# Optimization experiments

Hardware: AMD Instinct MI355X
Metric: run time of the kernel (lower is better)

Reference implementation:

```python
import jax, jax.numpy as jnp
import numpy as np

B, CLEN, QLEN, H = 32, 384, 64, 768


def _p(key, shape, scale=0.02):
    return jax.random.normal(key, shape, dtype=jnp.float32) * scale


def setup_inputs() -> dict:
    key = jax.random.key(0)
    ks = iter(jax.random.split(key, 64))
    d = {}
    d["c"] = jax.random.normal(next(ks), (B, CLEN, H), jnp.float32)
    d["q"] = jax.random.normal(next(ks), (B, QLEN, H), jnp.float32)
    d["w_att_c"] = _p(next(ks), (H,)); d["b_att_c"] = jnp.zeros((), jnp.float32)
    d["w_att_q"] = _p(next(ks), (H,)); d["b_att_q"] = jnp.zeros((), jnp.float32)
    d["w_att_cq"] = _p(next(ks), (H,)); d["b_att_cq"] = jnp.zeros((), jnp.float32)
    def add_lstm(prefix, in_dim):
        for dr in ("f", "b"):
            d[prefix + dr + "_wih"] = _p(next(ks), (4 * H, in_dim))
            d[prefix + dr + "_whh"] = _p(next(ks), (4 * H, H))
            d[prefix + dr + "_b"] = jnp.zeros((4 * H,), jnp.float32)  # b_ih + b_hh fused
    add_lstm("l1", 4 * H)  # modeling_LSTM1: input 4H
    add_lstm("l2", 2 * H)  # modeling_LSTM2: input 2H
    add_lstm("lo", 2 * H)  # output_LSTM: input 2H
    d["p1_wg"] = _p(next(ks), (4 * H,)); d["p1_bg"] = jnp.zeros((), jnp.float32)
    d["p1_wm"] = _p(next(ks), (2 * H,)); d["p1_bm"] = jnp.zeros((), jnp.float32)
    d["p2_wg"] = _p(next(ks), (4 * H,)); d["p2_bg"] = jnp.zeros((), jnp.float32)
    d["p2_wm"] = _p(next(ks), (2 * H,)); d["p2_bm"] = jnp.zeros((), jnp.float32)
    return d


def _lstm_dir(x, wih, whh, b):
    # single-direction LSTM, torch gate order (i, f, g, o)
    Bb, T, _ = x.shape
    Hh = whh.shape[1]
    xg = jnp.einsum("bti,gi->btg", x, wih) + b  # precompute input projections [B,T,4H]
    def step(carry, xt):
        h, cst = carry
        g = xt + h @ whh.T
        i, f, gg, o = jnp.split(g, 4, axis=-1)
        i = jax.nn.sigmoid(i); f = jax.nn.sigmoid(f)
        gg = jnp.tanh(gg); o = jax.nn.sigmoid(o)
        cst = f * cst + i * gg
        h = o * jnp.tanh(cst)
        return (h, cst), h
    init = (jnp.zeros((Bb, Hh), x.dtype), jnp.zeros((Bb, Hh), x.dtype))
    _, hs = jax.lax.scan(step, init, jnp.swapaxes(xg, 0, 1))
    return jnp.swapaxes(hs, 0, 1)


def _bilstm(x, fwih, fwhh, fb, bwih, bwhh, bb):
    hf = _lstm_dir(x, fwih, fwhh, fb)
    hb = _lstm_dir(x[:, ::-1], bwih, bwhh, bb)[:, ::-1]
    return jnp.concatenate([hf, hb], axis=-1)


def _forward(c, q,
             w_att_c, b_att_c, w_att_q, b_att_q, w_att_cq, b_att_cq,
             l1f_wih, l1f_whh, l1f_b, l1b_wih, l1b_whh, l1b_b,
             l2f_wih, l2f_whh, l2f_b, l2b_wih, l2b_whh, l2b_b,
             lof_wih, lof_whh, lof_b, lob_wih, lob_whh, lob_b,
             p1_wg, p1_bg, p1_wm, p1_bm, p2_wg, p2_bg, p2_wm, p2_bm):
    # --- att_flow_layer: trilinear similarity collapsed to a single einsum ---
    # original loops over q_len applying att_weight_cq(c * q_i); equivalent to:
    cq = jnp.einsum("bih,bjh,h->bij", c, q, w_att_cq) + b_att_cq  # [B,C,Q]
    s = (c @ w_att_c + b_att_c)[:, :, None] + (q @ w_att_q + b_att_q)[:, None, :] + cq
    a = jax.nn.softmax(s, axis=2)                       # attend context->query
    c2q = jnp.einsum("bij,bjh->bih", a, q)              # [B,C,H]
    b_w = jax.nn.softmax(jnp.max(s, axis=2), axis=1)    # [B,C]
    q2c = jnp.einsum("bi,bih->bh", b_w, c)[:, None, :]  # [B,1,H]
    g = jnp.concatenate([c, c2q, c * c2q, c * q2c], axis=-1)  # [B,C,8H? no, 4H]

    # --- modeling layers (two stacked biLSTMs) ---
    m1 = _bilstm(g, l1f_wih, l1f_whh, l1f_b, l1b_wih, l1b_whh, l1b_b)
    m = _bilstm(m1, l2f_wih, l2f_whh, l2f_b, l2b_wih, l2b_whh, l2b_b)

    # --- output layer ---
    p1 = (g @ p1_wg + p1_bg) + (m @ p1_wm + p1_bm)      # [B,C]
    m2 = _bilstm(m, lof_wih, lof_whh, lof_b, lob_wih, lob_whh, lob_b)
    p2 = (g @ p2_wg + p2_bg) + (m2 @ p2_wm + p2_bm)
    return p1, p2


def reference(c, q,
              w_att_c, b_att_c, w_att_q, b_att_q, w_att_cq, b_att_cq,
              l1f_wih, l1f_whh, l1f_b, l1b_wih, l1b_whh, l1b_b,
              l2f_wih, l2f_whh, l2f_b, l2b_wih, l2b_whh, l2b_b,
              lof_wih, lof_whh, lof_b, lob_wih, lob_whh, lob_b,
              p1_wg, p1_bg, p1_wm, p1_bm, p2_wg, p2_bg, p2_wm, p2_bm):
    return _forward(c, q,
                    w_att_c, b_att_c, w_att_q, b_att_q, w_att_cq, b_att_cq,
                    l1f_wih, l1f_whh, l1f_b, l1b_wih, l1b_whh, l1b_b,
                    l2f_wih, l2f_whh, l2f_b, l2b_wih, l2b_whh, l2b_b,
                    lof_wih, lof_whh, lof_b, lob_wih, lob_whh, lob_b,
                    p1_wg, p1_bg, p1_wm, p1_bm, p2_wg, p2_bg, p2_wm, p2_bm)
```

## Files before the change

### kernel.cpp

```cpp
#include <hip/hip_runtime.h>


typedef __bf16 bf16_t;
typedef __bf16 bf16x4 __attribute__((ext_vector_type(4)));
typedef __bf16 bf16x8 __attribute__((ext_vector_type(8)));
typedef float  f32x4  __attribute__((ext_vector_type(4)));
typedef unsigned long long ull;

#define TT 384

__device__ __forceinline__ void gload_lds16(const void* g, void* l) {
  __builtin_amdgcn_global_load_lds((const __attribute__((address_space(1))) void*)g,
                                   (__attribute__((address_space(3))) void*)l, 16, 0, 0);
}

__global__ void k_zeroE(unsigned* p) {
  int i = blockIdx.x * 256 + threadIdx.x;
  __hip_atomic_store(p + i, 0xFFFF0000u, __ATOMIC_RELAXED, __HIP_MEMORY_SCOPE_AGENT);
}

template<int BN, int EPI, int BSRC>
__global__ __launch_bounds__(256) void k_gemm(
    const bf16_t* __restrict__ A, const void* __restrict__ Bv, const void* __restrict__ Bv2,
    int nsplit, void* __restrict__ Cv,
    int M, int N, int K, long sAb, long sBb, long sCb,
    const float* __restrict__ rowb, const float* __restrict__ colb,
    const float* __restrict__ sb)
{
  constexpr int BM = 128, BK = 32;
  constexpr int NT = BN / 32;
  __shared__ bf16_t sA[BM * BK];
  __shared__ bf16_t sB[BN * BK];
  const int t    = threadIdx.x;
  const int lane = t & 63;
  const int wm   = (t >> 6) >> 1, wn = (t >> 6) & 1;
  const long bz  = blockIdx.z;
  const int nbase = blockIdx.y * BN;
  const bf16_t* Ab = A + bz * sAb + (long)blockIdx.x * BM * K;
  const bf16_t* Bb = nullptr;
  const float*  Bf = nullptr;
  if constexpr (BSRC == 0)
    Bb = (const bf16_t*)Bv + bz * sBb + (long)nbase * K;
  else
    Bf = (nbase < nsplit) ? ((const float*)Bv  + (long)nbase * K)
                          : ((const float*)Bv2 + (long)(nbase - nsplit) * K);

  const int r4 = t >> 2;
  const int kq = (t & 3) ^ ((r4 >> 1) & 3);

  f32x4 acc[4][NT];
  #pragma unroll
  for (int i = 0; i < 4; i++)
    #pragma unroll
    for (int j = 0; j < NT; j++) acc[i][j] = (f32x4){0.f, 0.f, 0.f, 0.f};

  const int mrow = lane & 15;
  const int fq   = lane >> 4;
  const int aswz = (fq ^ ((mrow >> 1) & 3)) * 8;

  for (int k0 = 0; k0 < K; k0 += BK) {
    __syncthreads();
    gload_lds16(Ab + (long)r4 * K + k0 + kq * 8,        (char*)sA + t * 16);
    gload_lds16(Ab + (long)(64 + r4) * K + k0 + kq * 8, (char*)sA + 4096 + t * 16);
    if constexpr (BSRC == 0) {
      gload_lds16(Bb + (long)r4 * K + k0 + kq * 8,        (char*)sB + t * 16);
      if constexpr (BN == 128)
        gload_lds16(Bb + (long)(64 + r4) * K + k0 + kq * 8, (char*)sB + 4096 + t * 16);
    } else {
      {
        f32x4 b0 = *(const f32x4*)(Bf + (long)r4 * K + k0 + kq * 8);
        f32x4 b1 = *(const f32x4*)(Bf + (long)r4 * K + k0 + kq * 8 + 4);
        bf16x8 bb;
        #pragma unroll
        for (int e = 0; e < 4; e++) { bb[e] = (bf16_t)b0[e]; bb[e + 4] = (bf16_t)b1[e]; }
        *(bf16x8*)((char*)sB + t * 16) = bb;
      }
      if constexpr (BN == 128) {
        f32x4 b0 = *(const f32x4*)(Bf + (long)(64 + r4) * K + k0 + kq * 8);
        f32x4 b1 = *(const f32x4*)(Bf + (long)(64 + r4) * K + k0 + kq * 8 + 4);
        bf16x8 bb;
        #pragma unroll
        for (int e = 0; e < 4; e++) { bb[e] = (bf16_t)b0[e]; bb[e + 4] = (bf16_t)b1[e]; }
        *(bf16x8*)((char*)sB + 4096 + t * 16) = bb;
      }
    }
    __syncthreads();

    bf16x8 af[4], bv[NT];
    #pragma unroll
    for (int mt = 0; mt < 4; mt++)
      af[mt] = *(const bf16x8*)(sA + (wm * 64 + mt * 16 + mrow) * 32 + aswz);
    #pragma unroll
    for (int nt = 0; nt < NT; nt++)
      bv[nt] = *(const bf16x8*)(sB + (wn * (BN / 2) + nt * 16 + mrow) * 32 + aswz);
    #pragma unroll
    for (int mt = 0; mt < 4; mt++)
      #pragma unroll
      for (int nt = 0; nt < NT; nt++)
        acc[mt][nt] = __builtin_amdgcn_mfma_f32_16x16x32_bf16(af[mt], bv[nt], acc[mt][nt], 0, 0, 0);
  }

  const int rbase = (lane >> 4) * 4;
  #pragma unroll
  for (int mt = 0; mt < 4; mt++)
    #pragma unroll
    for (int nt = 0; nt < NT; nt++)
      #pragma unroll
      for (int r = 0; r < 4; r++) {
        int grow = blockIdx.x * BM + wm * 64 + mt * 16 + rbase + r;
        int gcol = nbase + wn * (BN / 2) + nt * 16 + (lane & 15);
        if constexpr (EPI == 0) {
          ((bf16_t*)Cv)[bz * sCb + (long)grow * N + gcol] = (bf16_t)acc[mt][nt][r];
        } else {
          ((float*)Cv)[bz * sCb + (long)grow * N + gcol] =
              acc[mt][nt][r] + rowb[bz * M + grow] + colb[bz * N + gcol] + sb[0];
        }
      }
}

__global__ __launch_bounds__(512) void k_lstm(
    const bf16_t* __restrict__ xg, bf16_t* __restrict__ mout,
    unsigned* __restrict__ E,
    const float* __restrict__ whh_f, const float* __restrict__ whh_b,
    const float* __restrict__ bias_f, const float* __restrict__ bias_b,
    int tagbase)
{
  __shared__ bf16_t sH[16 * 776];
  __shared__ float  sG[4 * 544];
  const int t    = threadIdx.x;
  const int lane = t & 63;
  const int w    = t >> 6;
  const int g    = w & 3;
  const int ch   = w >> 2;
  const int blk  = blockIdx.x;
  const int dir  = blk / 48;
  const int qq   = blk - dir * 48;
  const int sl   = qq >> 1;
  const int bg   = qq & 1;
  const int j0   = sl * 32;
  const float* whh  = dir ? whh_b : whh_f;
  const float* bias = dir ? bias_b : bias_f;

  const int mrow = lane & 15;
  const int fq   = lane >> 4;

  bf16x8 bw[24];
  {
    const float* wrow = whh + (long)(g * 768 + j0 + ch * 16 + mrow) * 768 + fq * 8;
    #pragma unroll
    for (int kc = 0; kc < 24; kc++) {
      f32x4 v0 = *(const f32x4*)(wrow + kc * 32);
      f32x4 v1 = *(const f32x4*)(wrow + kc * 32 + 4);
      bf16x8 bb;
      #pragma unroll
      for (int e = 0; e < 4; e++) { bb[e] = (bf16_t)v0[e]; bb[e + 4] = (bf16_t)v1[e]; }
      bw[kc] = bb;
    }
  }

  const int b16 = t >> 5;
  const int jj  = t & 31;
  float bsv[4];
  #pragma unroll
  for (int gi = 0; gi < 4; gi++) bsv[gi] = bias[gi * 768 + j0 + jj];

  int soff[12];
  #pragma unroll
  for (int i = 0; i < 12; i++) {
    int e = i * 512 + t;
    soff[i] = (e / 384) * 1552 + (e % 384) * 4;
  }

  float cst = 0.f;
  const int aoff0 = mrow * 776 + fq * 8;
  const long xrow0 = (long)(bg * 16 + b16) * TT;

  for (int s = 0; s < TT; s++) {
    const int tc = dir ? (TT - 1 - s) : s;

    float xv[4];
    {
      long xr = (xrow0 + tc) * 6144 + dir * 3072 + j0 + jj;
      #pragma unroll
      for (int gi = 0; gi < 4; gi++) xv[gi] = (float)xg[xr + gi * 768];
    }

    if (s == 0) {
      for (int e = t; e < 1552; e += 512)
        *(f32x4*)((char*)sH + e * 16) = (f32x4){0.f, 0.f, 0.f, 0.f};
    } else {
      const unsigned want = (unsigned)(tagbase + s - 1);
      const int par = (s - 1) & 1;
      const ull* src = (const ull*)E + ((long)(par * 2 + dir) * 32 + bg * 16) * 384;
      ull qv[12];
      #pragma unroll
      for (int i = 0; i < 12; i++)
        qv[i] = __hip_atomic_load(src + i * 512 + t, __ATOMIC_RELAXED, __HIP_MEMORY_SCOPE_AGENT);
      for (;;) {
        unsigned bad = 0;
        #pragma unroll
        for (int i = 0; i < 12; i++) {
          unsigned lo = (unsigned)qv[i], hi = (unsigned)(qv[i] >> 32);
          if ((lo >> 16) != want || (hi >> 16) != want) bad |= 1u << i;
        }
        if (!bad) break;
        #pragma unroll
        for (int i = 0; i < 12; i++)
          if (bad & (1u << i))
            qv[i] = __hip_atomic_load(src + i * 512 + t, __ATOMIC_RELAXED, __HIP_MEMORY_SCOPE_AGENT);
      }
      #pragma unroll
      for (int i = 0; i < 12; i++) {
        ushort2 hh;
        hh.x = (unsigned short)qv[i];
        hh.y = (unsigned short)(qv[i] >> 32);
        *(ushort2*)((char*)sH + soff[i]) = hh;
      }
    }
    __syncthreads();

    f32x4 a0 = (f32x4){0.f, 0.f, 0.f, 0.f};
    f32x4 a1 = (f32x4){0.f, 0.f, 0.f, 0.f};
    #pragma unroll
    for (int kc = 0; kc < 24; kc += 2) {
      bf16x8 av0 = *(const bf16x8*)(sH + aoff0 + kc * 32);
      bf16x8 av1 = *(const bf16x8*)(sH + aoff0 + kc * 32 + 32);
      a0 = __builtin_amdgcn_mfma_f32_16x16x32_bf16(av0, bw[kc],     a0, 0, 0, 0);
      a1 = __builtin_amdgcn_mfma_f32_16x16x32_bf16(av1, bw[kc + 1], a1, 0, 0, 0);
    }
    #pragma unroll
    for (int r = 0; r < 4; r++)
      sG[g * 544 + (ch * 16 + mrow) * 17 + fq * 4 + r] = a0[r] + a1[r];
    __syncthreads();

    {
      float gi = sG[0 * 544 + jj * 17 + b16] + xv[0] + bsv[0];
      float gf = sG[1 * 544 + jj * 17 + b16] + xv[1] + bsv[1];
      float gg = sG[2 * 544 + jj * 17 + b16] + xv[2] + bsv[2];
      float go = sG[3 * 544 + jj * 17 + b16] + xv[3] + bsv[3];
      gi = 1.f / (1.f + __expf(-gi));
      gf = 1.f / (1.f + __expf(-gf));
      gg = 1.f - 2.f / (__expf(2.f * gg) + 1.f);
      go = 1.f / (1.f + __expf(-go));
      cst = gf * cst + gi * gg;
      float hv = go * (1.f - 2.f / (__expf(2.f * cst) + 1.f));
      union { bf16_t b; unsigned short u; } pk;
      pk.b = (bf16_t)hv;
      unsigned tag = (unsigned)(tagbase + s);
      long ed = ((long)((s & 1) * 2 + dir) * 32 + bg * 16 + b16) * 768 + j0 + jj;
      __hip_atomic_store(E + ed, (tag << 16) | pk.u,
                         __ATOMIC_RELAXED, __HIP_MEMORY_SCOPE_AGENT);
      mout[(xrow0 + tc) * 1536 + dir * 768 + j0 + jj] = pk.b;
    }
  }
}


__global__ __launch_bounds__(256) void k_pack(
    const float* __restrict__ c, const float* __restrict__ q,
    const float* __restrict__ wcq, bf16_t* __restrict__ cw, bf16_t* __restrict__ qb)
{
  int i = blockIdx.x * 256 + threadIdx.x;
  if (i < 9437184) {
    int h = i % 768;
    cw[i] = (bf16_t)(c[i] * wcq[h]);
  } else {
    int j = i - 9437184;
    qb[j] = (bf16_t)q[j];
  }
}

__global__ __launch_bounds__(256) void k_proj(
    const float* __restrict__ c, const float* __restrict__ q,
    const float* __restrict__ wc, const float* __restrict__ bc,
    const float* __restrict__ wq, const float* __restrict__ bq,
    float* __restrict__ projc, float* __restrict__ projq)
{
  int row  = blockIdx.x * 4 + (threadIdx.x >> 6);
  int lane = threadIdx.x & 63;
  const float *src, *w;
  bool isC = row < 12288;
  if (isC) { src = c + (long)row * 768;          w = wc; }
  else     { src = q + (long)(row - 12288) * 768; w = wq; }
  float a = 0.f;
  for (int k = lane * 4; k < 768; k += 256) {
    f32x4 v = *(const f32x4*)(src + k);
    f32x4 wv = *(const f32x4*)(w + k);
    a += v[0]*wv[0] + v[1]*wv[1] + v[2]*wv[2] + v[3]*wv[3];
  }
  for (int m = 32; m; m >>= 1) a += __shfl_xor(a, m);
  if (lane == 0) {
    if (isC) projc[row] = a + bc[0];
    else     projq[row - 12288] = a + bq[0];
  }
}

__global__ __launch_bounds__(256) void k_smax_j(
    const float* __restrict__ s, bf16_t* __restrict__ a, float* __restrict__ smax)
{
  int row  = blockIdx.x * 4 + (threadIdx.x >> 6);
  int lane = threadIdx.x & 63;
  float v = s[(long)row * 64 + lane];
  float mx = v;
  for (int m = 32; m; m >>= 1) mx = fmaxf(mx, __shfl_xor(mx, m));
  float p = __expf(v - mx);
  float sum = p;
  for (int m = 32; m; m >>= 1) sum += __shfl_xor(sum, m);
  a[(long)row * 64 + lane] = (bf16_t)(p / sum);
  if (lane == 0) smax[row] = mx;
}

__global__ __launch_bounds__(384) void k_smax_i(
    const float* __restrict__ smax, float* __restrict__ bw)
{
  __shared__ float red[8];
  int b = blockIdx.x, t = threadIdx.x;
  int lane = t & 63, wv = t >> 6;
  float v = smax[b * 384 + t];
  float mx = v;
  for (int m = 32; m; m >>= 1) mx = fmaxf(mx, __shfl_xor(mx, m));
  if (lane == 0) red[wv] = mx;
  __syncthreads();
  float gm = red[0];
  #pragma unroll
  for (int i = 1; i < 6; i++) gm = fmaxf(gm, red[i]);
  float p = __expf(v - gm);
  float sm = p;
  for (int m = 32; m; m >>= 1) sm += __shfl_xor(sm, m);
  __syncthreads();
  if (lane == 0) red[wv] = sm;
  __syncthreads();
  float tot = red[0];
  #pragma unroll
  for (int i = 1; i < 6; i++) tot += red[i];
  bw[b * 384 + t] = p / tot;
}

__global__ __launch_bounds__(256) void k_q2c(
    const float* __restrict__ bw, const float* __restrict__ c, float* __restrict__ q2c)
{
  int b = blockIdx.y;
  int h = blockIdx.x * 256 + threadIdx.x;
  const float* cb = c + (long)b * 384 * 768;
  float acc = 0.f;
  for (int i = 0; i < 384; i++) acc += bw[b * 384 + i] * cb[(long)i * 768 + h];
  q2c[b * 768 + h] = acc;
}

__global__ __launch_bounds__(256) void k_tq(
    const bf16_t* __restrict__ qb, bf16_t* __restrict__ qT)
{
  __shared__ bf16_t sT[64][72];
  int b = blockIdx.y, hc = blockIdx.x, t = threadIdx.x;
  {
    int j = t >> 2, h0 = (t & 3) * 16;
    const bf16_t* src = qb + (long)(b * 64 + j) * 768 + hc * 64 + h0;
    *(bf16x8*)&sT[j][h0]     = *(const bf16x8*)(src);
    *(bf16x8*)&sT[j][h0 + 8] = *(const bf16x8*)(src + 8);
  }
  __syncthreads();
  {
    int h = t >> 2, j0 = (t & 3) * 16;
    bf16x8 o0, o1;
    #pragma unroll
    for (int e = 0; e < 8; e++) { o0[e] = sT[j0 + e][h]; o1[e] = sT[j0 + 8 + e][h]; }
    bf16_t* dst = qT + (long)(b * 768 + hc * 64 + h) * 64 + j0;
    *(bf16x8*)dst       = o0;
    *(bf16x8*)(dst + 8) = o1;
  }
}

__global__ __launch_bounds__(256) void k_buildg(
    const float* __restrict__ c, const bf16_t* __restrict__ c2q,
    const float* __restrict__ q2c, bf16_t* __restrict__ g)
{
  int i = blockIdx.x * 256 + threadIdx.x;
  int h = i % 768;
  int row = i / 768;
  int b = row / 384;
  float cv  = c[i];
  float cqv = (float)c2q[i];
  float qcv = q2c[b * 768 + h];
  bf16_t* gr = g + (long)row * 3072;
  gr[h]        = (bf16_t)cv;
  gr[768 + h]  = c2q[i];
  gr[1536 + h] = (bf16_t)(cv * cqv);
  gr[2304 + h] = (bf16_t)(cv * qcv);
}

__global__ __launch_bounds__(256) void k_headsg(
    const bf16_t* __restrict__ g, const float* __restrict__ w1, const float* __restrict__ w2,
    float* __restrict__ pg1, float* __restrict__ pg2)
{
  int row  = blockIdx.x * 4 + (threadIdx.x >> 6);
  int lane = threadIdx.x & 63;
  float a1 = 0.f, a2 = 0.f;
  const bf16_t* gr = g + (long)row * 3072;
  for (int k = lane * 8; k < 3072; k += 512) {
    bf16x8 v = *(const bf16x8*)(gr + k);
    f32x4 wa = *(const f32x4*)(w1 + k), wb = *(const f32x4*)(w1 + k + 4);
    f32x4 xa = *(const f32x4*)(w2 + k), xb = *(const f32x4*)(w2 + k + 4);
    #pragma unroll
    for (int e = 0; e < 4; e++) {
      a1 += (float)v[e] * wa[e] + (float)v[e + 4] * wb[e];
      a2 += (float)v[e] * xa[e] + (float)v[e + 4] * xb[e];
    }
  }
  for (int m_ = 32; m_; m_ >>= 1) { a1 += __shfl_xor(a1, m_); a2 += __shfl_xor(a2, m_); }
  if (lane == 0) { pg1[row] = a1; pg2[row] = a2; }
}

__global__ __launch_bounds__(256) void k_headsm(
    const bf16_t* __restrict__ m, const float* __restrict__ wm,
    const float* __restrict__ pg, const float* __restrict__ bg,
    const float* __restrict__ bm, float* __restrict__ out)
{
  int row  = blockIdx.x * 4 + (threadIdx.x >> 6);
  int lane = threadIdx.x & 63;
  float a = 0.f;
  const bf16_t* mr = m + (long)row * 1536;
  for (int k = lane * 8; k < 1536; k += 512) {
    bf16x8 v = *(const bf16x8*)(mr + k);
    f32x4 wa = *(const f32x4*)(wm + k), wb = *(const f32x4*)(wm + k + 4);
    #pragma unroll
    for (int e = 0; e < 4; e++) a += (float)v[e] * wa[e] + (float)v[e + 4] * wb[e];
  }
  for (int m_ = 32; m_; m_ >>= 1) a += __shfl_xor(a, m_);
  if (lane == 0) out[row] = pg[row] + a + bg[0] + bm[0];
}


extern "C" void kernel_launch(void* const* d_in, const int* in_sizes, int n_in,
                              void* d_out, int out_size, void* d_ws, size_t ws_size,
                              hipStream_t stream)
{
  (void)in_sizes; (void)n_in; (void)out_size; (void)ws_size;
  const float* c    = (const float*)d_in[0];
  const float* q    = (const float*)d_in[1];
  const float* wac  = (const float*)d_in[2];
  const float* bac  = (const float*)d_in[3];
  const float* waq  = (const float*)d_in[4];
  const float* baq  = (const float*)d_in[5];
  const float* wacq = (const float*)d_in[6];
  const float* bacq = (const float*)d_in[7];
  const float* l1f_wih = (const float*)d_in[8];
  const float* l1f_whh = (const float*)d_in[9];
  const float* l1f_b   = (const float*)d_in[10];
  const float* l1b_wih = (const float*)d_in[11];
  const float* l1b_whh = (const float*)d_in[12];
  const float* l1b_b   = (const float*)d_in[13];
  const float* l2f_wih = (const float*)d_in[14];
  const float* l2f_whh = (const float*)d_in[15];
  const float* l2f_b   = (const float*)d_in[16];
  const float* l2b_wih = (const float*)d_in[17];
  const float* l2b_whh = (const float*)d_in[18];
  const float* l2b_b   = (const float*)d_in[19];
  const float* lof_wih = (const float*)d_in[20];
  const float* lof_whh = (const float*)d_in[21];
  const float* lof_b   = (const float*)d_in[22];
  const float* lob_wih = (const float*)d_in[23];
  const float* lob_whh = (const float*)d_in[24];
  const float* lob_b   = (const float*)d_in[25];
  const float* p1wg = (const float*)d_in[26];
  const float* p1bg = (const float*)d_in[27];
  const float* p1wm = (const float*)d_in[28];
  const float* p1bm = (const float*)d_in[29];
  const float* p2wg = (const float*)d_in[30];
  const float* p2bg = (const float*)d_in[31];
  const float* p2wm = (const float*)d_in[32];
  const float* p2bm = (const float*)d_in[33];

  char* ws = (char*)d_ws;
  bf16_t* g_bf = (bf16_t*)ws;
  bf16_t* mA   = (bf16_t*)ws;
  bf16_t* mB   = (bf16_t*)(ws + 37748736L);
  bf16_t* m2   = (bf16_t*)ws;
  char*   xgc  = ws + 75497472L;
  bf16_t* xg   = (bf16_t*)xgc;
  bf16_t* cw  = (bf16_t*)xgc;
  bf16_t* qb  = (bf16_t*)(xgc + 18874368L);
  bf16_t* qT  = (bf16_t*)(xgc + 22020096L);
  float*  sS  = (float*) (xgc + 25165824L);
  bf16_t* aP  = (bf16_t*)(xgc + 28311552L);
  bf16_t* c2q = (bf16_t*)(xgc + 29884416L);
  char* tail = ws + 226492416L;
  float*    projc = (float*)tail;
  float*    projq = (float*)(tail + 49152);
  float*    smax  = (float*)(tail + 57344);
  float*    bw    = (float*)(tail + 106496);
  float*    q2c   = (float*)(tail + 155648);
  float*    pg1   = (float*)(tail + 253952);
  float*    pg2   = (float*)(tail + 303104);
  unsigned* E     = (unsigned*)(tail + 352256);

  k_zeroE<<<768, 256, 0, stream>>>(E);

  k_pack<<<43008, 256, 0, stream>>>(c, q, wacq, cw, qb);
  k_proj<<<3584, 256, 0, stream>>>(c, q, wac, bac, waq, baq, projc, projq);
  k_gemm<64,1,0><<<dim3(3,1,32), 256, 0, stream>>>(cw, qb, nullptr, 1<<30, sS,
      384, 64, 768, (long)384*768, (long)64*768, (long)384*64, projc, projq, bacq);
  k_smax_j<<<3072, 256, 0, stream>>>(sS, aP, smax);
  k_smax_i<<<32, 384, 0, stream>>>(smax, bw);
  k_q2c<<<dim3(3,32), 256, 0, stream>>>(bw, c, q2c);
  k_tq<<<dim3(12,32), 256, 0, stream>>>(qb, qT);
  k_gemm<64,0,0><<<dim3(3,12,32), 256, 0, stream>>>(aP, qT, nullptr, 1<<30, c2q,
      384, 768, 64, (long)384*64, (long)768*64, (long)384*768, nullptr, nullptr, nullptr);
  k_buildg<<<36864, 256, 0, stream>>>(c, c2q, q2c, g_bf);
  k_headsg<<<3072, 256, 0, stream>>>(g_bf, p1wg, p2wg, pg1, pg2);

  k_gemm<128,0,1><<<dim3(96,48,1), 256, 0, stream>>>(g_bf, l1f_wih, l1b_wih, 3072, xg,
      12288, 6144, 3072, 0, 0, 0, nullptr, nullptr, nullptr);
  k_lstm<<<96, 512, 0, stream>>>(xg, mA, E, l1f_whh, l1b_whh, l1f_b, l1b_b, 0);

  k_gemm<128,0,1><<<dim3(96,48,1), 256, 0, stream>>>(mA, l2f_wih, l2b_wih, 3072, xg,
      12288, 6144, 1536, 0, 0, 0, nullptr, nullptr, nullptr);
  k_lstm<<<96, 512, 0, stream>>>(xg, mB, E, l2f_whh, l2b_whh, l2f_b, l2b_b, 384);
  k_headsm<<<3072, 256, 0, stream>>>(mB, p1wm, pg1, p1bg, p1bm, (float*)d_out);

  k_gemm<128,0,1><<<dim3(96,48,1), 256, 0, stream>>>(mB, lof_wih, lob_wih, 3072, xg,
      12288, 6144, 1536, 0, 0, 0, nullptr, nullptr, nullptr);
  k_lstm<<<96, 512, 0, stream>>>(xg, m2, E, lof_whh, lob_whh, lof_b, lob_b, 768);
  k_headsm<<<3072, 256, 0, stream>>>(m2, p2wm, pg2, p2bg, p2bm, (float*)d_out + 12288);
}
```

Measured before the change: 6.563 ms.

## Interleave four direction/batch-group LSTM phases per block with prefetched handoff loads

Result: slower. 10.66 ms (+62.5%).

```diff
diff --git a/kernel.cpp b/kernel.cpp
--- a/kernel.cpp
+++ b/kernel.cpp
@@ -12,6 +12,12 @@
 __device__ __forceinline__ void gload_lds16(const void* g, void* l) {
   __builtin_amdgcn_global_load_lds((const __attribute__((address_space(1))) void*)g,
                                    (__attribute__((address_space(3))) void*)l, 16, 0, 0);
+}
+
+__device__ __forceinline__ void wg_barrier_lds() {
+  asm volatile("s_waitcnt lgkmcnt(0)" ::: "memory");
+  __builtin_amdgcn_s_barrier();
+  asm volatile("" ::: "memory");
 }
 
 __global__ void k_zeroE(unsigned* p) {
@@ -118,6 +124,88 @@
       }
 }
 
+
+#define LSTM_PHASE(D, BGc, CST, QV, ID, IB, IPAR)                                  \
+  {                                                                                \
+    const int tc = (D) ? (TT - 1 - s) : s;                                         \
+    float xv0 = 0.f, xv1 = 0.f, xv2 = 0.f, xv3 = 0.f;                              \
+    if (t < 256) {                                                                 \
+      long xr = ((long)((BGc) * 16 + b16e) * TT + tc) * 6144 + (D) * 3072 + j0 + jje; \
+      xv0 = (float)xg[xr];        xv1 = (float)xg[xr + 768];                       \
+      xv2 = (float)xg[xr + 1536]; xv3 = (float)xg[xr + 2304];                      \
+    }                                                                              \
+    if (s == 0) {                                                                  \
+      if ((D) == 0 && (BGc) == 0) {                                                \
+        for (int e = t; e < 1552; e += 512)                                        \
+          *(f32x4*)((char*)sH + e * 16) = (f32x4){0.f, 0.f, 0.f, 0.f};             \
+      }                                                                            \
+    } else {                                                                       \
+      const unsigned want = (unsigned)(tagbase + s - 1);                           \
+      const ull* rsrc = (const ull*)E + ((long)(((s - 1) & 1) * 2 + (D)) * 32 + (BGc) * 16) * 384; \
+      for (;;) {                                                                   \
+        unsigned bad = 0;                                                          \
+        _Pragma("unroll")                                                          \
+        for (int i = 0; i < 12; i++) {                                             \
+          unsigned lo = (unsigned)QV[i], hi = (unsigned)(QV[i] >> 32);             \
+          if ((lo >> 16) != want || (hi >> 16) != want) bad |= 1u << i;            \
+        }                                                                          \
+        if (!bad) break;                                                           \
+        _Pragma("unroll")                                                          \
+        for (int i = 0; i < 12; i++)                                               \
+          if (bad & (1u << i))                                                     \
+            QV[i] = __hip_atomic_load(rsrc + i * 512 + t, __ATOMIC_RELAXED, __HIP_MEMORY_SCOPE_AGENT); \
+      }                                                                            \
+      _Pragma("unroll")                                                            \
+      for (int i = 0; i < 12; i++) {                                               \
+        ushort2 hh;                                                                \
+        hh.x = (unsigned short)QV[i];                                              \
+        hh.y = (unsigned short)(QV[i] >> 32);                                      \
+        *(ushort2*)((char*)sH + soff[i]) = hh;                                     \
+      }                                                                            \
+    }                                                                              \
+    {                                                                              \
+      const ull* isrc = (const ull*)E + ((long)((IPAR) * 2 + (ID)) * 32 + (IB) * 16) * 384; \
+      _Pragma("unroll")                                                            \
+      for (int i = 0; i < 12; i++)                                                 \
+        QV[i] = __hip_atomic_load(isrc + i * 512 + t, __ATOMIC_RELAXED, __HIP_MEMORY_SCOPE_AGENT); \
+    }                                                                              \
+    wg_barrier_lds();                                                              \
+    if (wd == (D)) {                                                               \
+      f32x4 a0 = (f32x4){0.f, 0.f, 0.f, 0.f};                                      \
+      f32x4 a1 = (f32x4){0.f, 0.f, 0.f, 0.f};                                      \
+      _Pragma("unroll")                                                            \
+      for (int kc = 0; kc < 24; kc += 2) {                                         \
+        bf16x8 av0 = *(const bf16x8*)(sH + aoff0 + kc * 32);                       \
+        bf16x8 av1 = *(const bf16x8*)(sH + aoff0 + kc * 32 + 32);                  \
+        a0 = __builtin_amdgcn_mfma_f32_16x16x32_bf16(av0, bw[kc],     a0, 0, 0, 0);\
+        a1 = __builtin_amdgcn_mfma_f32_16x16x32_bf16(av1, bw[kc + 1], a1, 0, 0, 0);\
+      }                                                                            \
+      _Pragma("unroll")                                                            \
+      for (int r = 0; r < 4; r++)                                                  \
+        sG[g * 272 + mrow * 17 + fq * 4 + r] = a0[r] + a1[r];                      \
+    }                                                                              \
+    wg_barrier_lds();                                                              \
+    if (t < 256) {                                                                 \
+      float gv0 = sG[0 * 272 + jje * 17 + b16e] + xv0 + ((D) ? bsb0 : bsf0);       \
+      float gv1 = sG[1 * 272 + jje * 17 + b16e] + xv1 + ((D) ? bsb1 : bsf1);       \
+      float gv2 = sG[2 * 272 + jje * 17 + b16e] + xv2 + ((D) ? bsb2 : bsf2);       \
+      float gv3 = sG[3 * 272 + jje * 17 + b16e] + xv3 + ((D) ? bsb3 : bsf3);       \
+      gv0 = 1.f / (1.f + __expf(-gv0));                                            \
+      gv1 = 1.f / (1.f + __expf(-gv1));                                            \
+      gv2 = 1.f - 2.f / (__expf(2.f * gv2) + 1.f);                                 \
+      gv3 = 1.f / (1.f + __expf(-gv3));                                            \
+      CST = gv1 * CST + gv0 * gv2;                                                 \
+      float hv = gv3 * (1.f - 2.f / (__expf(2.f * CST) + 1.f));                    \
+      union { bf16_t b; unsigned short u; } pk;                                    \
+      pk.b = (bf16_t)hv;                                                           \
+      unsigned tag = (unsigned)(tagbase + s);                                      \
+      long ed = ((long)((s & 1) * 2 + (D)) * 32 + (BGc) * 16 + b16e) * 768 + j0 + jje; \
+      __hip_atomic_store(E + ed, (tag << 16) | pk.u,                               \
+                         __ATOMIC_RELAXED, __HIP_MEMORY_SCOPE_AGENT);              \
+      mout[((long)((BGc) * 16 + b16e) * TT + tc) * 1536 + (D) * 768 + j0 + jje] = pk.b; \
+    }                                                                              \
+  }
+
 __global__ __launch_bounds__(512) void k_lstm(
     const bf16_t* __restrict__ xg, bf16_t* __restrict__ mout,
     unsigned* __restrict__ E,
@@ -126,27 +214,22 @@
     int tagbase)
 {
   __shared__ bf16_t sH[16 * 776];
-  __shared__ float  sG[4 * 544];
+  __shared__ float  sG[4 * 272];
   const int t    = threadIdx.x;
   const int lane = t & 63;
   const int w    = t >> 6;
   const int g    = w & 3;
-  const int ch   = w >> 2;
-  const int blk  = blockIdx.x;
-  const int dir  = blk / 48;
-  const int qq   = blk - dir * 48;
-  const int sl   = qq >> 1;
-  const int bg   = qq & 1;
-  const int j0   = sl * 32;
-  const float* whh  = dir ? whh_b : whh_f;
-  const float* bias = dir ? bias_b : bias_f;
-
+  const int wd   = w >> 2;
+  const int j0   = blockIdx.x * 16;
   const int mrow = lane & 15;
   const int fq   = lane >> 4;
-
+  const int jje  = t & 15;
+  const int b16e = (t >> 4) & 15;
+
+  const float* whh = wd ? whh_b : whh_f;
   bf16x8 bw[24];
   {
-    const float* wrow = whh + (long)(g * 768 + j0 + ch * 16 + mrow) * 768 + fq * 8;
+    const float* wrow = whh + (long)(g * 768 + j0 + mrow) * 768 + fq * 8;
     #pragma unroll
     for (int kc = 0; kc < 24; kc++) {
       f32x4 v0 = *(const f32x4*)(wrow + kc * 32);
@@ -158,11 +241,14 @@
     }
   }
 
-  const int b16 = t >> 5;
-  const int jj  = t & 31;
-  float bsv[4];
-  #pragma unroll
-  for (int gi = 0; gi < 4; gi++) bsv[gi] = bias[gi * 768 + j0 + jj];
+  const float bsf0 = bias_f[0 * 768 + j0 + jje];
+  const float bsf1 = bias_f[1 * 768 + j0 + jje];
+  const float bsf2 = bias_f[2 * 768 + j0 + jje];
+  const float bsf3 = bias_f[3 * 768 + j0 + jje];
+  const float bsb0 = bias_b[0 * 768 + j0 + jje];
+  const float bsb1 = bias_b[1 * 768 + j0 + jje];
+  const float bsb2 = bias_b[2 * 768 + j0 + jje];
+  const float bsb3 = bias_b[3 * 768 + j0 + jje];
 
   int soff[12];
   #pragma unroll
@@ -171,87 +257,16 @@
     soff[i] = (e / 384) * 1552 + (e % 384) * 4;
   }
 
-  float cst = 0.f;
   const int aoff0 = mrow * 776 + fq * 8;
-  const long xrow0 = (long)(bg * 16 + b16) * TT;
+
+  float cst00 = 0.f, cst01 = 0.f, cst10 = 0.f, cst11 = 0.f;
+  ull qvA[12] = {}, qvB[12] = {};
 
   for (int s = 0; s < TT; s++) {
-    const int tc = dir ? (TT - 1 - s) : s;
-
-    float xv[4];
-    {
-      long xr = (xrow0 + tc) * 6144 + dir * 3072 + j0 + jj;
-      #pragma unroll
-      for (int gi = 0; gi < 4; gi++) xv[gi] = (float)xg[xr + gi * 768];
-    }
-
-    if (s == 0) {
-      for (int e = t; e < 1552; e += 512)
-        *(f32x4*)((char*)sH + e * 16) = (f32x4){0.f, 0.f, 0.f, 0.f};
-    } else {
-      const unsigned want = (unsigned)(tagbase + s - 1);
-      const int par = (s - 1) & 1;
-      const ull* src = (const ull*)E + ((long)(par * 2 + dir) * 32 + bg * 16) * 384;
-      ull qv[12];
-      #pragma unroll
-      for (int i = 0; i < 12; i++)
-        qv[i] = __hip_atomic_load(src + i * 512 + t, __ATOMIC_RELAXED, __HIP_MEMORY_SCOPE_AGENT);
-      for (;;) {
-        unsigned bad = 0;
-        #pragma unroll
-        for (int i = 0; i < 12; i++) {
-          unsigned lo = (unsigned)qv[i], hi = (unsigned)(qv[i] >> 32);
-          if ((lo >> 16) != want || (hi >> 16) != want) bad |= 1u << i;
-        }
-        if (!bad) break;
-        #pragma unroll
-        for (int i = 0; i < 12; i++)
-          if (bad & (1u << i))
-            qv[i] = __hip_atomic_load(src + i * 512 + t, __ATOMIC_RELAXED, __HIP_MEMORY_SCOPE_AGENT);
-      }
-      #pragma unroll
-      for (int i = 0; i < 12; i++) {
-        ushort2 hh;
-        hh.x = (unsigned short)qv[i];
-        hh.y = (unsigned short)(qv[i] >> 32);
-        *(ushort2*)((char*)sH + soff[i]) = hh;
-      }
-    }
-    __syncthreads();
-
-    f32x4 a0 = (f32x4){0.f, 0.f, 0.f, 0.f};
-    f32x4 a1 = (f32x4){0.f, 0.f, 0.f, 0.f};
-    #pragma unroll
-    for (int kc = 0; kc < 24; kc += 2) {
-      bf16x8 av0 = *(const bf16x8*)(sH + aoff0 + kc * 32);
-      bf16x8 av1 = *(const bf16x8*)(sH + aoff0 + kc * 32 + 32);
-      a0 = __builtin_amdgcn_mfma_f32_16x16x32_bf16(av0, bw[kc],     a0, 0, 0, 0);
-      a1 = __builtin_amdgcn_mfma_f32_16x16x32_bf16(av1, bw[kc + 1], a1, 0, 0, 0);
-    }
-    #pragma unroll
-    for (int r = 0; r < 4; r++)
-      sG[g * 544 + (ch * 16 + mrow) * 17 + fq * 4 + r] = a0[r] + a1[r];
-    __syncthreads();
-
-    {
-      float gi = sG[0 * 544 + jj * 17 + b16] + xv[0] + bsv[0];
-      float gf = sG[1 * 544 + jj * 17 + b16] + xv[1] + bsv[1];
-      float gg = sG[2 * 544 + jj * 17 + b16] + xv[2] + bsv[2];
-      float go = sG[3 * 544 + jj * 17 + b16] + xv[3] + bsv[3];
-      gi = 1.f / (1.f + __expf(-gi));
-      gf = 1.f / (1.f + __expf(-gf));
-      gg = 1.f - 2.f / (__expf(2.f * gg) + 1.f);
-      go = 1.f / (1.f + __expf(-go));
-      cst = gf * cst + gi * gg;
-      float hv = go * (1.f - 2.f / (__expf(2.f * cst) + 1.f));
-      union { bf16_t b; unsigned short u; } pk;
-      pk.b = (bf16_t)hv;
-      unsigned tag = (unsigned)(tagbase + s);
-      long ed = ((long)((s & 1) * 2 + dir) * 32 + bg * 16 + b16) * 768 + j0 + jj;
-      __hip_atomic_store(E + ed, (tag << 16) | pk.u,
-                         __ATOMIC_RELAXED, __HIP_MEMORY_SCOPE_AGENT);
-      mout[(xrow0 + tc) * 1536 + dir * 768 + j0 + jj] = pk.b;
-    }
+    LSTM_PHASE(0, 0, cst00, qvA, 1, 0, ((s - 1) & 1))
+    LSTM_PHASE(0, 1, cst01, qvB, 1, 1, ((s - 1) & 1))
+    LSTM_PHASE(1, 0, cst10, qvA, 0, 0, (s & 1))
+    LSTM_PHASE(1, 1, cst11, qvB, 0, 1, (s & 1))
   }
 }
 
@@ -510,15 +525,15 @@
 
   k_gemm<128,0,1><<<dim3(96,48,1), 256, 0, stream>>>(g_bf, l1f_wih, l1b_wih, 3072, xg,
       12288, 6144, 3072, 0, 0, 0, nullptr, nullptr, nullptr);
-  k_lstm<<<96, 512, 0, stream>>>(xg, mA, E, l1f_whh, l1b_whh, l1f_b, l1b_b, 0);
+  k_lstm<<<48, 512, 0, stream>>>(xg, mA, E, l1f_whh, l1b_whh, l1f_b, l1b_b, 0);
 
   k_gemm<128,0,1><<<dim3(96,48,1), 256, 0, stream>>>(mA, l2f_wih, l2b_wih, 3072, xg,
       12288, 6144, 1536, 0, 0, 0, nullptr, nullptr, nullptr);
-  k_lstm<<<96, 512, 0, stream>>>(xg, mB, E, l2f_whh, l2b_whh, l2f_b, l2b_b, 384);
+  k_lstm<<<48, 512, 0, stream>>>(xg, mB, E, l2f_whh, l2b_whh, l2f_b, l2b_b, 384);
   k_headsm<<<3072, 256, 0, stream>>>(mB, p1wm, pg1, p1bg, p1bm, (float*)d_out);
 
   k_gemm<128,0,1><<<dim3(96,48,1), 256, 0, stream>>>(mB, lof_wih, lob_wih, 3072, xg,
       12288, 6144, 1536, 0, 0, 0, nullptr, nullptr, nullptr);
-  k_lstm<<<96, 512, 0, stream>>>(xg, m2, E, lof_whh, lob_whh, lof_b, lob_b, 768);
+  k_lstm<<<48, 512, 0, stream>>>(xg, m2, E, lof_whh, lob_whh, lof_b, lob_b, 768);
   k_headsm<<<3072, 256, 0, stream>>>(m2, p2wm, pg2, p2bg, p2bm, (float*)d_out + 12288);
 }
```

## Halve LSTM block count with 1024-thread blocks, prefetch inputs, pack stores

Applied to the files above, without the earlier changes.

After: 10.51 ms. +60.1%, slower.

```diff
diff --git a/kernel.cpp b/kernel.cpp
--- a/kernel.cpp
+++ b/kernel.cpp
@@ -12,6 +12,12 @@
 __device__ __forceinline__ void gload_lds16(const void* g, void* l) {
   __builtin_amdgcn_global_load_lds((const __attribute__((address_space(1))) void*)g,
                                    (__attribute__((address_space(3))) void*)l, 16, 0, 0);
+}
+
+__device__ __forceinline__ void wg_barrier_lds() {
+  asm volatile("s_waitcnt lgkmcnt(0)" ::: "memory");
+  __builtin_amdgcn_s_barrier();
+  asm volatile("" ::: "memory");
 }
 
 __global__ void k_zeroE(unsigned* p) {
@@ -118,7 +124,7 @@
       }
 }
 
-__global__ __launch_bounds__(512) void k_lstm(
+__global__ __launch_bounds__(1024) void k_lstm(
     const bf16_t* __restrict__ xg, bf16_t* __restrict__ mout,
     unsigned* __restrict__ E,
     const float* __restrict__ whh_f, const float* __restrict__ whh_b,
@@ -126,18 +132,18 @@
     int tagbase)
 {
   __shared__ bf16_t sH[16 * 776];
-  __shared__ float  sG[4 * 544];
+  __shared__ float  sG[4 * 64 * 17];
   const int t    = threadIdx.x;
   const int lane = t & 63;
   const int w    = t >> 6;
   const int g    = w & 3;
   const int ch   = w >> 2;
   const int blk  = blockIdx.x;
-  const int dir  = blk / 48;
-  const int qq   = blk - dir * 48;
+  const int dir  = blk / 24;
+  const int qq   = blk - dir * 24;
   const int sl   = qq >> 1;
   const int bg   = qq & 1;
-  const int j0   = sl * 32;
+  const int j0   = sl * 64;
   const float* whh  = dir ? whh_b : whh_f;
   const float* bias = dir ? bias_b : bias_f;
 
@@ -158,66 +164,77 @@
     }
   }
 
-  const int b16 = t >> 5;
-  const int jj  = t & 31;
+  const int jje  = t & 63;
+  const int b16e = t >> 6;
   float bsv[4];
   #pragma unroll
-  for (int gi = 0; gi < 4; gi++) bsv[gi] = bias[gi * 768 + j0 + jj];
-
-  int soff[12];
+  for (int gi = 0; gi < 4; gi++) bsv[gi] = bias[gi * 768 + j0 + jje];
+
+  int soff[6];
   #pragma unroll
-  for (int i = 0; i < 12; i++) {
-    int e = i * 512 + t;
+  for (int i = 0; i < 6; i++) {
+    int e = i * 1024 + t;
     soff[i] = (e / 384) * 1552 + (e % 384) * 4;
   }
 
   float cst = 0.f;
   const int aoff0 = mrow * 776 + fq * 8;
-  const long xrow0 = (long)(bg * 16 + b16) * TT;
+  const long xrow0 = (long)(bg * 16 + b16e) * TT;
+
+  float xc[4], xn[4];
+  {
+    int tc0 = dir ? (TT - 1) : 0;
+    long xr = (xrow0 + tc0) * 6144 + dir * 3072 + j0 + jje;
+    #pragma unroll
+    for (int gi = 0; gi < 4; gi++) xn[gi] = (float)xg[xr + gi * 768];
+  }
 
   for (int s = 0; s < TT; s++) {
     const int tc = dir ? (TT - 1 - s) : s;
 
-    float xv[4];
+    #pragma unroll
+    for (int gi = 0; gi < 4; gi++) xc[gi] = xn[gi];
     {
-      long xr = (xrow0 + tc) * 6144 + dir * 3072 + j0 + jj;
+      int sn = (s + 1 < TT) ? s + 1 : s;
+      int tcn = dir ? (TT - 1 - sn) : sn;
+      long xr = (xrow0 + tcn) * 6144 + dir * 3072 + j0 + jje;
       #pragma unroll
-      for (int gi = 0; gi < 4; gi++) xv[gi] = (float)xg[xr + gi * 768];
+      for (int gi = 0; gi < 4; gi++) xn[gi] = (float)xg[xr + gi * 768];
     }
 
     if (s == 0) {
-      for (int e = t; e < 1552; e += 512)
+      for (int e = t; e < 1552; e += 1024)
         *(f32x4*)((char*)sH + e * 16) = (f32x4){0.f, 0.f, 0.f, 0.f};
     } else {
       const unsigned want = (unsigned)(tagbase + s - 1);
       const int par = (s - 1) & 1;
       const ull* src = (const ull*)E + ((long)(par * 2 + dir) * 32 + bg * 16) * 384;
-      ull qv[12];
+      ull qv[6];
       #pragma unroll
-      for (int i = 0; i < 12; i++)
-        qv[i] = __hip_atomic_load(src + i * 512 + t, __ATOMIC_RELAXED, __HIP_MEMORY_SCOPE_AGENT);
+      for (int i = 0; i < 6; i++)
+        qv[i] = __hip_atomic_load(src + i * 1024 + t, __ATOMIC_RELAXED, __HIP_MEMORY_SCOPE_AGENT);
       for (;;) {
         unsigned bad = 0;
         #pragma unroll
-        for (int i = 0; i < 12; i++) {
+        for (int i = 0; i < 6; i++) {
           unsigned lo = (unsigned)qv[i], hi = (unsigned)(qv[i] >> 32);
           if ((lo >> 16) != want || (hi >> 16) != want) bad |= 1u << i;
         }
         if (!bad) break;
         #pragma unroll
-        for (int i = 0; i < 12; i++)
+        for (int i = 0; i < 6; i++)
           if (bad & (1u << i))
-            qv[i] = __hip_atomic_load(src + i * 512 + t, __ATOMIC_RELAXED, __HIP_MEMORY_SCOPE_AGENT);
+            qv[i] = __hip_atomic_load(src + i * 1024 + t, __ATOMIC_RELAXED, __HIP_MEMORY_SCOPE_AGENT);
       }
       #pragma unroll
-      for (int i = 0; i < 12; i++) {
+      for (int i = 0; i < 6; i++) {
         ushort2 hh;
         hh.x = (unsigned short)qv[i];
         hh.y = (unsigned short)(qv[i] >> 32);
         *(ushort2*)((char*)sH + soff[i]) = hh;
       }
     }
-    __syncthreads();
+    wg_barrier_lds();
 
     f32x4 a0 = (f32x4){0.f, 0.f, 0.f, 0.f};
     f32x4 a1 = (f32x4){0.f, 0.f, 0.f, 0.f};
@@ -230,27 +247,32 @@
     }
     #pragma unroll
     for (int r = 0; r < 4; r++)
-      sG[g * 544 + (ch * 16 + mrow) * 17 + fq * 4 + r] = a0[r] + a1[r];
-    __syncthreads();
+      sG[g * 1088 + (ch * 16 + mrow) * 17 + fq * 4 + r] = a0[r] + a1[r];
+    wg_barrier_lds();
 
     {
-      float gi = sG[0 * 544 + jj * 17 + b16] + xv[0] + bsv[0];
-      float gf = sG[1 * 544 + jj * 17 + b16] + xv[1] + bsv[1];
-      float gg = sG[2 * 544 + jj * 17 + b16] + xv[2] + bsv[2];
-      float go = sG[3 * 544 + jj * 17 + b16] + xv[3] + bsv[3];
-      gi = 1.f / (1.f + __expf(-gi));
-      gf = 1.f / (1.f + __expf(-gf));
-      gg = 1.f - 2.f / (__expf(2.f * gg) + 1.f);
-      go = 1.f / (1.f + __expf(-go));
-      cst = gf * cst + gi * gg;
-      float hv = go * (1.f - 2.f / (__expf(2.f * cst) + 1.f));
+      float gv0 = sG[0 * 1088 + jje * 17 + b16e] + xc[0] + bsv[0];
+      float gv1 = sG[1 * 1088 + jje * 17 + b16e] + xc[1] + bsv[1];
+      float gv2 = sG[2 * 1088 + jje * 17 + b16e] + xc[2] + bsv[2];
+      float gv3 = sG[3 * 1088 + jje * 17 + b16e] + xc[3] + bsv[3];
+      gv0 = 1.f / (1.f + __expf(-gv0));
+      gv1 = 1.f / (1.f + __expf(-gv1));
+      gv2 = 1.f - 2.f / (__expf(2.f * gv2) + 1.f);
+      gv3 = 1.f / (1.f + __expf(-gv3));
+      cst = gv1 * cst + gv0 * gv2;
+      float hv = gv3 * (1.f - 2.f / (__expf(2.f * cst) + 1.f));
       union { bf16_t b; unsigned short u; } pk;
       pk.b = (bf16_t)hv;
       unsigned tag = (unsigned)(tagbase + s);
-      long ed = ((long)((s & 1) * 2 + dir) * 32 + bg * 16 + b16) * 768 + j0 + jj;
-      __hip_atomic_store(E + ed, (tag << 16) | pk.u,
-                         __ATOMIC_RELAXED, __HIP_MEMORY_SCOPE_AGENT);
-      mout[(xrow0 + tc) * 1536 + dir * 768 + j0 + jj] = pk.b;
+      unsigned myd = (tag << 16) | pk.u;
+      unsigned od  = (unsigned)__shfl_xor((int)myd, 1);
+      if ((t & 1) == 0) {
+        long ed = ((long)((s & 1) * 2 + dir) * 32 + bg * 16 + b16e) * 768 + j0 + jje;
+        __hip_atomic_store((ull*)E + (ed >> 1), (ull)myd | ((ull)od << 32),
+                           __ATOMIC_RELAXED, __HIP_MEMORY_SCOPE_AGENT);
+        unsigned mo = (unsigned)pk.u | ((od & 0xFFFFu) << 16);
+        *(unsigned*)(mout + (xrow0 + tc) * 1536 + dir * 768 + j0 + jje) = mo;
+      }
     }
   }
 }
@@ -510,15 +532,15 @@
 
   k_gemm<128,0,1><<<dim3(96,48,1), 256, 0, stream>>>(g_bf, l1f_wih, l1b_wih, 3072, xg,
       12288, 6144, 3072, 0, 0, 0, nullptr, nullptr, nullptr);
-  k_lstm<<<96, 512, 0, stream>>>(xg, mA, E, l1f_whh, l1b_whh, l1f_b, l1b_b, 0);
+  k_lstm<<<48, 1024, 0, stream>>>(xg, mA, E, l1f_whh, l1b_whh, l1f_b, l1b_b, 0);
 
   k_gemm<128,0,1><<<dim3(96,48,1), 256, 0, stream>>>(mA, l2f_wih, l2b_wih, 3072, xg,
       12288, 6144, 1536, 0, 0, 0, nullptr, nullptr, nullptr);
-  k_lstm<<<96, 512, 0, stream>>>(xg, mB, E, l2f_whh, l2b_whh, l2f_b, l2b_b, 384);
+  k_lstm<<<48, 1024, 0, stream>>>(xg, mB, E, l2f_whh, l2b_whh, l2f_b, l2b_b, 384);
   k_headsm<<<3072, 256, 0, stream>>>(mB, p1wm, pg1, p1bg, p1bm, (float*)d_out);
 
   k_gemm<128,0,1><<<dim3(96,48,1), 256, 0, stream>>>(mB, lof_wih, lob_wih, 3072, xg,
       12288, 6144, 1536, 0, 0, 0, nullptr, nullptr, nullptr);
-  k_lstm<<<96, 512, 0, stream>>>(xg, m2, E, lof_whh, lob_whh, lof_b, lob_b, 768);
+  k_lstm<<<48, 1024, 0, stream>>>(xg, m2, E, lof_whh, lob_whh, lof_b, lob_b, 768);
   k_headsm<<<3072, 256, 0, stream>>>(m2, p2wm, pg2, p2bg, p2bm, (float*)d_out + 12288);
 }
```

## Replace per-element tagged hidden-state exchange with per-wave flags and packed data

Applied to the files above, without the earlier changes.

Result: slower. 8.310 ms (+26.6%).

```diff
diff --git a/kernel.cpp b/kernel.cpp
--- a/kernel.cpp
+++ b/kernel.cpp
@@ -14,9 +14,15 @@
                                    (__attribute__((address_space(3))) void*)l, 16, 0, 0);
 }
 
+__device__ __forceinline__ void wg_barrier_lds() {
+  asm volatile("s_waitcnt lgkmcnt(0)" ::: "memory");
+  __builtin_amdgcn_s_barrier();
+  asm volatile("" ::: "memory");
+}
+
 __global__ void k_zeroE(unsigned* p) {
   int i = blockIdx.x * 256 + threadIdx.x;
-  __hip_atomic_store(p + i, 0xFFFF0000u, __ATOMIC_RELAXED, __HIP_MEMORY_SCOPE_AGENT);
+  __hip_atomic_store(p + i, 0xFFFFFFFFu, __ATOMIC_RELAXED, __HIP_MEMORY_SCOPE_AGENT);
 }
 
 template<int BN, int EPI, int BSRC>
@@ -126,7 +132,7 @@
     int tagbase)
 {
   __shared__ bf16_t sH[16 * 776];
-  __shared__ float  sG[4 * 544];
+  __shared__ float  sG[4 * 272];
   const int t    = threadIdx.x;
   const int lane = t & 63;
   const int w    = t >> 6;
@@ -144,6 +150,9 @@
   const int mrow = lane & 15;
   const int fq   = lane >> 4;
 
+  unsigned* Es = E;
+  unsigned* Ed = E + 1536;
+
   bf16x8 bw[24];
   {
     const float* wrow = whh + (long)(g * 768 + j0 + ch * 16 + mrow) * 768 + fq * 8;
@@ -164,11 +173,11 @@
   #pragma unroll
   for (int gi = 0; gi < 4; gi++) bsv[gi] = bias[gi * 768 + j0 + jj];
 
-  int soff[12];
+  int soff[6];
   #pragma unroll
-  for (int i = 0; i < 12; i++) {
+  for (int i = 0; i < 6; i++) {
     int e = i * 512 + t;
-    soff[i] = (e / 384) * 1552 + (e % 384) * 4;
+    soff[i] = (e / 192) * 1552 + (e % 192) * 8;
   }
 
   float cst = 0.f;
@@ -177,13 +186,6 @@
 
   for (int s = 0; s < TT; s++) {
     const int tc = dir ? (TT - 1 - s) : s;
-
-    float xv[4];
-    {
-      long xr = (xrow0 + tc) * 6144 + dir * 3072 + j0 + jj;
-      #pragma unroll
-      for (int gi = 0; gi < 4; gi++) xv[gi] = (float)xg[xr + gi * 768];
-    }
 
     if (s == 0) {
       for (int e = t; e < 1552; e += 512)
@@ -191,33 +193,37 @@
     } else {
       const unsigned want = (unsigned)(tagbase + s - 1);
       const int par = (s - 1) & 1;
-      const ull* src = (const ull*)E + ((long)(par * 2 + dir) * 32 + bg * 16) * 384;
-      ull qv[12];
+      {
+        const unsigned* sp = Es + ((par * 2 + dir) * 2 + bg) * 192;
+        for (;;) {
+          unsigned s0 = __hip_atomic_load(sp + lane,       __ATOMIC_RELAXED, __HIP_MEMORY_SCOPE_AGENT);
+          unsigned s1 = __hip_atomic_load(sp + 64 + lane,  __ATOMIC_RELAXED, __HIP_MEMORY_SCOPE_AGENT);
+          unsigned s2 = __hip_atomic_load(sp + 128 + lane, __ATOMIC_RELAXED, __HIP_MEMORY_SCOPE_AGENT);
+          if (__all(s0 == want && s1 == want && s2 == want)) break;
+          __builtin_amdgcn_s_sleep(1);
+        }
+      }
+      asm volatile("" ::: "memory");
+      {
+        const ull* dq = (const ull*)Ed + ((long)(par * 2 + dir) * 32 + bg * 16) * 192;
+        ull qv[6];
+        #pragma unroll
+        for (int i = 0; i < 6; i++)
+          qv[i] = __hip_atomic_load(dq + i * 512 + t, __ATOMIC_RELAXED, __HIP_MEMORY_SCOPE_AGENT);
+        #pragma unroll
+        for (int i = 0; i < 6; i++)
+          *(ull*)((char*)sH + soff[i]) = qv[i];
+      }
+    }
+
+    float xv[4];
+    {
+      long xr = (xrow0 + tc) * 6144 + dir * 3072 + j0 + jj;
       #pragma unroll
-      for (int i = 0; i < 12; i++)
-        qv[i] = __hip_atomic_load(src + i * 512 + t, __ATOMIC_RELAXED, __HIP_MEMORY_SCOPE_AGENT);
-      for (;;) {
-        unsigned bad = 0;
-        #pragma unroll
-        for (int i = 0; i < 12; i++) {
-          unsigned lo = (unsigned)qv[i], hi = (unsigned)(qv[i] >> 32);
-          if ((lo >> 16) != want || (hi >> 16) != want) bad |= 1u << i;
-        }
-        if (!bad) break;
-        #pragma unroll
-        for (int i = 0; i < 12; i++)
-          if (bad & (1u << i))
-            qv[i] = __hip_atomic_load(src + i * 512 + t, __ATOMIC_RELAXED, __HIP_MEMORY_SCOPE_AGENT);
-      }
-      #pragma unroll
-      for (int i = 0; i < 12; i++) {
-        ushort2 hh;
-        hh.x = (unsigned short)qv[i];
-        hh.y = (unsigned short)(qv[i] >> 32);
-        *(ushort2*)((char*)sH + soff[i]) = hh;
-      }
-    }
-    __syncthreads();
+      for (int gi = 0; gi < 4; gi++) xv[gi] = (float)xg[xr + gi * 768];
+    }
+
+    wg_barrier_lds();
 
     f32x4 a0 = (f32x4){0.f, 0.f, 0.f, 0.f};
     f32x4 a1 = (f32x4){0.f, 0.f, 0.f, 0.f};
@@ -230,27 +236,37 @@
     }
     #pragma unroll
     for (int r = 0; r < 4; r++)
-      sG[g * 544 + (ch * 16 + mrow) * 17 + fq * 4 + r] = a0[r] + a1[r];
-    __syncthreads();
+      sG[g * 272 + (ch * 16 + mrow) * 17 + fq * 4 + r] = a0[r] + a1[r];
+    wg_barrier_lds();
 
     {
-      float gi = sG[0 * 544 + jj * 17 + b16] + xv[0] + bsv[0];
-      float gf = sG[1 * 544 + jj * 17 + b16] + xv[1] + bsv[1];
-      float gg = sG[2 * 544 + jj * 17 + b16] + xv[2] + bsv[2];
-      float go = sG[3 * 544 + jj * 17 + b16] + xv[3] + bsv[3];
-      gi = 1.f / (1.f + __expf(-gi));
-      gf = 1.f / (1.f + __expf(-gf));
-      gg = 1.f - 2.f / (__expf(2.f * gg) + 1.f);
-      go = 1.f / (1.f + __expf(-go));
-      cst = gf * cst + gi * gg;
-      float hv = go * (1.f - 2.f / (__expf(2.f * cst) + 1.f));
+      float gv0 = sG[0 * 272 + jj * 17 + b16] + xv[0] + bsv[0];
+      float gv1 = sG[1 * 272 + jj * 17 + b16] + xv[1] + bsv[1];
+      float gv2 = sG[2 * 272 + jj * 17 + b16] + xv[2] + bsv[2];
+      float gv3 = sG[3 * 272 + jj * 17 + b16] + xv[3] + bsv[3];
+      gv0 = 1.f / (1.f + __expf(-gv0));
+      gv1 = 1.f / (1.f + __expf(-gv1));
+      gv2 = 1.f - 2.f / (__expf(2.f * gv2) + 1.f);
+      gv3 = 1.f / (1.f + __expf(-gv3));
+      cst = gv1 * cst + gv0 * gv2;
+      float hv = gv3 * (1.f - 2.f / (__expf(2.f * cst) + 1.f));
       union { bf16_t b; unsigned short u; } pk;
       pk.b = (bf16_t)hv;
-      unsigned tag = (unsigned)(tagbase + s);
-      long ed = ((long)((s & 1) * 2 + dir) * 32 + bg * 16 + b16) * 768 + j0 + jj;
-      __hip_atomic_store(E + ed, (tag << 16) | pk.u,
+      unsigned myd = (unsigned)pk.u;
+      unsigned od  = (unsigned)__shfl_xor((int)myd, 1);
+      if ((t & 1) == 0) {
+        unsigned mo = myd | (od << 16);
+        long di = ((long)((s & 1) * 2 + dir) * 32 + bg * 16 + b16) * 768 + j0 + jj;
+        __hip_atomic_store(Ed + (di >> 1), mo,
+                           __ATOMIC_RELAXED, __HIP_MEMORY_SCOPE_AGENT);
+        *(unsigned*)(mout + (xrow0 + tc) * 1536 + dir * 768 + j0 + jj) = mo;
+      }
+    }
+    asm volatile("s_waitcnt vmcnt(0)" ::: "memory");
+    if (lane == 0) {
+      __hip_atomic_store(Es + (((s & 1) * 2 + dir) * 2 + bg) * 192 + sl * 8 + w,
+                         (unsigned)(tagbase + s),
                          __ATOMIC_RELAXED, __HIP_MEMORY_SCOPE_AGENT);
-      mout[(xrow0 + tc) * 1536 + dir * 768 + j0 + jj] = pk.b;
     }
   }
 }
@@ -493,7 +509,7 @@
   float*    pg2   = (float*)(tail + 303104);
   unsigned* E     = (unsigned*)(tail + 352256);
 
-  k_zeroE<<<768, 256, 0, stream>>>(E);
+  k_zeroE<<<6, 256, 0, stream>>>(E);
 
   k_pack<<<43008, 256, 0, stream>>>(c, q, wacq, cw, qb);
   k_proj<<<3584, 256, 0, stream>>>(c, q, wac, bac, waq, baq, projc, projq);
```
